# Kernel tuning notes

Hardware: AMD Instinct MI355X
Metric: run time of the kernel (lower is better)

The kernel has to match this reference:

```python
import jax, jax.numpy as jnp
import numpy as np

N_BITS = 4
SIZE_SCALE = 8 // N_BITS  # 2 int4 values per byte
MASK = (1 << N_BITS) - 1  # 0xF

OC, IC = 8192, 8192
B = 64


def setup_inputs() -> dict:
    key = jax.random.key(0)
    k_in, k_w, k_d, k_z, k_b = jax.random.split(key, 5)
    input = jax.random.normal(k_in, (B, IC), dtype=jnp.float32)
    # packed uint8 weight buffer: [OC // SIZE_SCALE, IC]; stored as int32 with byte values
    weight_packed = jax.random.randint(k_w, (OC // SIZE_SCALE, IC), 0, 256, dtype=jnp.int32)
    # per-output-channel affine quant params
    delta = jax.random.uniform(k_d, (OC,), dtype=jnp.float32) * 0.01 + 1e-4
    zero_point = jax.random.uniform(k_z, (OC,), dtype=jnp.float32) * MASK
    bias = jax.random.normal(k_b, (OC,), dtype=jnp.float32)
    return {"input": input, "weight_packed": weight_packed, "delta": delta,
            "zero_point": zero_point, "bias": bias}


def _dequantize(weight_packed, delta, zero_point):
    # Bit-unpack: each byte holds SIZE_SCALE values of N_BITS each, packed along
    # the output-channel dim (dim 0), low nibble first.
    parts = [ (weight_packed >> (N_BITS * i)) & MASK for i in range(SIZE_SCALE) ]
    w_int = jnp.concatenate(parts, axis=0)               # [OC, IC] int
    # Affine dequant, per output channel: w = (q - zp) * delta
    w = (w_int.astype(jnp.float32) - zero_point[:, None]) * delta[:, None]
    return w


def reference(input, weight_packed, delta, zero_point, bias):
    # use_weight_quant=True, use_act_quant=False (defaults in the module)
    w = _dequantize(weight_packed, delta, zero_point)    # [OC, IC]
    out = jnp.dot(input, w.T) + bias                     # F.linear
    return out
```

## Files before the change

### kernel.cpp

```cpp
#include <hip/hip_runtime.h>

constexpr int BATCH = 64;
constexpr int IC    = 8192;
constexpr int OC    = 8192;
constexpr int OCH   = 4096;
constexpr int KSPLIT = 4;
constexpr int KPER  = IC / KSPLIT;
constexpr int BK    = 64;
constexpr int LDK   = BK + 8;

typedef __bf16 bf16x8 __attribute__((ext_vector_type(8)));
typedef float  f32x4  __attribute__((ext_vector_type(4)));

static __device__ __forceinline__ unsigned short f2bf(float f) {
    unsigned u = __float_as_uint(f);
    u += 0x7FFFu + ((u >> 16) & 1u);
    return (unsigned short)(u >> 16);
}

static __device__ __forceinline__ unsigned short ibf(int n) {
    return (unsigned short)(__float_as_uint((float)n) >> 16);
}

__global__ __launch_bounds__(256) void prep_kernel(
    const float* __restrict__ in, unsigned short* __restrict__ Abf,
    float* __restrict__ S)
{
    const int b = blockIdx.x;
    const int t = threadIdx.x;
    const float* row = in + (size_t)b * IC;
    unsigned short* orow = Abf + (size_t)b * IC;

    float sum = 0.f;
#pragma unroll
    for (int i = 0; i < IC / 1024; ++i) {
        const int c = i * 1024 + t * 4;
        const float4 v = *(const float4*)(row + c);
        sum += (v.x + v.y) + (v.z + v.w);
        ushort4 o = make_ushort4(f2bf(v.x), f2bf(v.y), f2bf(v.z), f2bf(v.w));
        *(ushort4*)(orow + c) = o;
    }
#pragma unroll
    for (int off = 32; off > 0; off >>= 1) sum += __shfl_down(sum, off);

    __shared__ float red[4];
    if ((t & 63) == 0) red[t >> 6] = sum;
    __syncthreads();
    if (t == 0) S[b] = (red[0] + red[1]) + (red[2] + red[3]);
}

__global__ __launch_bounds__(256) void gemm_kernel(
    const unsigned short* __restrict__ Abf,
    const int* __restrict__ wp,
    const float* __restrict__ delta,
    const float* __restrict__ zp,
    const float* __restrict__ bias,
    const float* __restrict__ S,
    float* __restrict__ out)
{
    __shared__ unsigned short lA[64 * LDK];
    __shared__ unsigned short lW[64 * LDK];

    const int t    = threadIdx.x;
    const int wave = t >> 6;
    const int lane = t & 63;
    const int lm   = lane & 15;
    const int lq   = lane >> 4;

    const int nt = blockIdx.x & 127;
    const int ks = blockIdx.x >> 7;
    const int r0 = nt * 32;
    const int kb0 = ks * KPER;

    f32x4 acc[4];
    const f32x4 zero4 = {0.f, 0.f, 0.f, 0.f};
#pragma unroll
    for (int i = 0; i < 4; ++i) acc[i] = zero4;

    const int uAr = t >> 3, uAs = t & 7;
    const int uWr = t >> 4, uWs = t & 15;

    for (int kk = 0; kk < KPER; kk += BK) {
        const int kb = kb0 + kk;
        const int4 a0 = *(const int4*)(Abf + (size_t)uAr        * IC + kb + uAs * 8);
        const int4 a1 = *(const int4*)(Abf + (size_t)(uAr + 32) * IC + kb + uAs * 8);
        const int4 w0 = *(const int4*)(wp  + (size_t)(r0 + uWr)      * IC + kb + uWs * 4);
        const int4 w1 = *(const int4*)(wp  + (size_t)(r0 + uWr + 16) * IC + kb + uWs * 4);

        __syncthreads();

        *(int4*)(&lA[uAr        * LDK + uAs * 8]) = a0;
        *(int4*)(&lA[(uAr + 32) * LDK + uAs * 8]) = a1;

        {
            ushort4 lo = make_ushort4(ibf(w0.x & 15), ibf(w0.y & 15),
                                      ibf(w0.z & 15), ibf(w0.w & 15));
            ushort4 hi = make_ushort4(ibf((w0.x >> 4) & 15), ibf((w0.y >> 4) & 15),
                                      ibf((w0.z >> 4) & 15), ibf((w0.w >> 4) & 15));
            *(ushort4*)(&lW[uWr        * LDK + uWs * 4]) = lo;
            *(ushort4*)(&lW[(uWr + 32) * LDK + uWs * 4]) = hi;
        }
        {
            ushort4 lo = make_ushort4(ibf(w1.x & 15), ibf(w1.y & 15),
                                      ibf(w1.z & 15), ibf(w1.w & 15));
            ushort4 hi = make_ushort4(ibf((w1.x >> 4) & 15), ibf((w1.y >> 4) & 15),
                                      ibf((w1.z >> 4) & 15), ibf((w1.w >> 4) & 15));
            *(ushort4*)(&lW[(uWr + 16) * LDK + uWs * 4]) = lo;
            *(ushort4*)(&lW[(uWr + 48) * LDK + uWs * 4]) = hi;
        }

        __syncthreads();

#pragma unroll
        for (int s = 0; s < 2; ++s) {
            const int kc = s * 32 + lq * 8;
            const bf16x8 bfrg = *(const bf16x8*)(&lW[(wave * 16 + lm) * LDK + kc]);
#pragma unroll
            for (int mt = 0; mt < 4; ++mt) {
                const bf16x8 afrg = *(const bf16x8*)(&lA[(mt * 16 + lm) * LDK + kc]);
                acc[mt] = __builtin_amdgcn_mfma_f32_16x16x32_bf16(afrg, bfrg, acc[mt], 0, 0, 0);
            }
        }
    }

    const int cr = wave * 16 + lm;
    const int ch = (cr < 32) ? (r0 + cr) : (OCH + r0 + (cr - 32));
    const float d  = delta[ch];
    const float dz = d * zp[ch];
    const float bi = bias[ch];
    constexpr float inv_split = 1.f / (float)KSPLIT;

#pragma unroll
    for (int mt = 0; mt < 4; ++mt) {
#pragma unroll
        for (int r = 0; r < 4; ++r) {
            const int m = mt * 16 + lq * 4 + r;
            const float res = d * acc[mt][r] + (bi - dz * S[m]) * inv_split;
            atomicAdd(out + (size_t)m * OC + ch, res);
        }
    }
}

extern "C" void kernel_launch(void* const* d_in, const int* in_sizes, int n_in,
                              void* d_out, int out_size, void* d_ws, size_t ws_size,
                              hipStream_t stream) {
    const float* input = (const float*)d_in[0];
    const int*   wpk   = (const int*)d_in[1];
    const float* delta = (const float*)d_in[2];
    const float* zp    = (const float*)d_in[3];
    const float* bias  = (const float*)d_in[4];
    float* out = (float*)d_out;

    unsigned short* Abf = (unsigned short*)d_ws;
    float* S = (float*)((char*)d_ws + (size_t)BATCH * IC * 2);

    hipMemsetAsync(d_out, 0, (size_t)out_size * sizeof(float), stream);
    prep_kernel<<<dim3(BATCH), dim3(256), 0, stream>>>(input, Abf, S);
    gemm_kernel<<<dim3(128 * KSPLIT), dim3(256), 0, stream>>>(Abf, wpk, delta, zp, bias, S, out);
}
```

Before: 218.9 us.

## Prefetch next K tile into registers, double split-K, pack bf16 conversion with perm

Global loads for the next K tile are issued right after the LDS stores, so memory latency overlaps with the MFMA loop instead of stalling it. Split-K goes from 4 to 8 to launch more blocks for this small-batch GEMM, with launch bounds set to request 4 blocks per CU. Nibble-to-bf16 conversion now packs two values per v_perm and uses wider 16-byte LDS stores with a new thread-to-tile mapping. The cost is twice as many atomic adds on the output and a wasted extra prefetch on the final iteration.

New measurement: 227.1 us. 3.7% more time.

```diff
diff --git a/kernel.cpp b/kernel.cpp
--- a/kernel.cpp
+++ b/kernel.cpp
@@ -4,9 +4,10 @@
 constexpr int IC    = 8192;
 constexpr int OC    = 8192;
 constexpr int OCH   = 4096;
-constexpr int KSPLIT = 4;
+constexpr int KSPLIT = 8;
 constexpr int KPER  = IC / KSPLIT;
 constexpr int BK    = 64;
+constexpr int NITER = KPER / BK;
 constexpr int LDK   = BK + 8;
 
 typedef __bf16 bf16x8 __attribute__((ext_vector_type(8)));
@@ -18,8 +19,10 @@
     return (unsigned short)(u >> 16);
 }
 
-static __device__ __forceinline__ unsigned short ibf(int n) {
-    return (unsigned short)(__float_as_uint((float)n) >> 16);
+static __device__ __forceinline__ unsigned pack2bf(int n0, int n1) {
+    unsigned f0 = __float_as_uint((float)n0);
+    unsigned f1 = __float_as_uint((float)n1);
+    return __builtin_amdgcn_perm(f1, f0, 0x07060302u);
 }
 
 __global__ __launch_bounds__(256) void prep_kernel(
@@ -49,7 +52,7 @@
     if (t == 0) S[b] = (red[0] + red[1]) + (red[2] + red[3]);
 }
 
-__global__ __launch_bounds__(256) void gemm_kernel(
+__global__ __launch_bounds__(256, 4) void gemm_kernel(
     const unsigned short* __restrict__ Abf,
     const int* __restrict__ wp,
     const float* __restrict__ delta,
@@ -67,9 +70,9 @@
     const int lm   = lane & 15;
     const int lq   = lane >> 4;
 
-    const int nt = blockIdx.x & 127;
-    const int ks = blockIdx.x >> 7;
-    const int r0 = nt * 32;
+    const int nt  = blockIdx.x & 127;
+    const int ks  = blockIdx.x >> 7;
+    const int r0  = nt * 32;
     const int kb0 = ks * KPER;
 
     f32x4 acc[4];
@@ -77,39 +80,44 @@
 #pragma unroll
     for (int i = 0; i < 4; ++i) acc[i] = zero4;
 
-    const int uAr = t >> 3, uAs = t & 7;
-    const int uWr = t >> 4, uWs = t & 15;
+    const int uAr = t >> 2, uAc = (t & 3) * 16;
+    const int uWr = t >> 3, uWc = (t & 7) * 8;
 
-    for (int kk = 0; kk < KPER; kk += BK) {
-        const int kb = kb0 + kk;
-        const int4 a0 = *(const int4*)(Abf + (size_t)uAr        * IC + kb + uAs * 8);
-        const int4 a1 = *(const int4*)(Abf + (size_t)(uAr + 32) * IC + kb + uAs * 8);
-        const int4 w0 = *(const int4*)(wp  + (size_t)(r0 + uWr)      * IC + kb + uWs * 4);
-        const int4 w1 = *(const int4*)(wp  + (size_t)(r0 + uWr + 16) * IC + kb + uWs * 4);
+    const unsigned short* pA = Abf + (size_t)uAr * IC + kb0 + uAc;
+    const int*            pW = wp  + (size_t)(r0 + uWr) * IC + kb0 + uWc;
+
+    int4 a0 = *(const int4*)(pA);
+    int4 a1 = *(const int4*)(pA + 8);
+    int4 w0 = *(const int4*)(pW);
+    int4 w1 = *(const int4*)(pW + 4);
+
+    for (int it = 0; it < NITER; ++it) {
+        __syncthreads();
+
+        *(int4*)(&lA[uAr * LDK + uAc])     = a0;
+        *(int4*)(&lA[uAr * LDK + uAc + 8]) = a1;
+
+        int4 lo, hi;
+        lo.x = pack2bf( w0.x       & 15,  w0.y       & 15);
+        lo.y = pack2bf( w0.z       & 15,  w0.w       & 15);
+        lo.z = pack2bf( w1.x       & 15,  w1.y       & 15);
+        lo.w = pack2bf( w1.z       & 15,  w1.w       & 15);
+        hi.x = pack2bf((w0.x >> 4) & 15, (w0.y >> 4) & 15);
+        hi.y = pack2bf((w0.z >> 4) & 15, (w0.w >> 4) & 15);
+        hi.z = pack2bf((w1.x >> 4) & 15, (w1.y >> 4) & 15);
+        hi.w = pack2bf((w1.z >> 4) & 15, (w1.w >> 4) & 15);
+        *(int4*)(&lW[uWr        * LDK + uWc]) = lo;
+        *(int4*)(&lW[(uWr + 32) * LDK + uWc]) = hi;
 
         __syncthreads();
 
-        *(int4*)(&lA[uAr        * LDK + uAs * 8]) = a0;
-        *(int4*)(&lA[(uAr + 32) * LDK + uAs * 8]) = a1;
-
         {
-            ushort4 lo = make_ushort4(ibf(w0.x & 15), ibf(w0.y & 15),
-                                      ibf(w0.z & 15), ibf(w0.w & 15));
-            ushort4 hi = make_ushort4(ibf((w0.x >> 4) & 15), ibf((w0.y >> 4) & 15),
-                                      ibf((w0.z >> 4) & 15), ibf((w0.w >> 4) & 15));
-            *(ushort4*)(&lW[uWr        * LDK + uWs * 4]) = lo;
-            *(ushort4*)(&lW[(uWr + 32) * LDK + uWs * 4]) = hi;
+            const int koff = ((it + 1) & (NITER - 1)) * BK;
+            a0 = *(const int4*)(pA + koff);
+            a1 = *(const int4*)(pA + koff + 8);
+            w0 = *(const int4*)(pW + koff);
+            w1 = *(const int4*)(pW + koff + 4);
         }
-        {
-            ushort4 lo = make_ushort4(ibf(w1.x & 15), ibf(w1.y & 15),
-                                      ibf(w1.z & 15), ibf(w1.w & 15));
-            ushort4 hi = make_ushort4(ibf((w1.x >> 4) & 15), ibf((w1.y >> 4) & 15),
-                                      ibf((w1.z >> 4) & 15), ibf((w1.w >> 4) & 15));
-            *(ushort4*)(&lW[(uWr + 16) * LDK + uWs * 4]) = lo;
-            *(ushort4*)(&lW[(uWr + 48) * LDK + uWs * 4]) = hi;
-        }
-
-        __syncthreads();
 
 #pragma unroll
         for (int s = 0; s < 2; ++s) {
```
